# Kernel optimization log

Measured on AMD Instinct MI355X. Metric: run time of the kernel, lower is better.

Reference implementation:

```python
import jax, jax.numpy as jnp
import numpy as np

PASSES = 6
S = 2           # numEdgeSets
D = 256         # inputLayerSize
OUT = 10        # outputLayerSize
HID = 80
B, N, E = 4, 10000, 160000


def _leaky(x):
    return jax.nn.leaky_relu(x, negative_slope=0.01)


def setup_inputs() -> dict:
    key = jax.random.key(0)
    ks = jax.random.split(key, 18)
    sc = 0.05
    return {
        "nodes": jax.random.normal(ks[0], (B, N, D), jnp.float32),
        "edges": jax.random.randint(ks[1], (B, S, E, 2), 0, N, jnp.int32),
        "problem_type": jax.random.uniform(ks[2], (B, 1), jnp.float32),
        # GRUCell params (torch layout: [3D, D] for ih and hh)
        "gru_w_ih": jax.random.normal(ks[3], (3 * D, D), jnp.float32) * sc,
        "gru_w_hh": jax.random.normal(ks[4], (3 * D, D), jnp.float32) * sc,
        "gru_b_ih": jax.random.normal(ks[5], (3 * D,), jnp.float32) * sc,
        "gru_b_hh": jax.random.normal(ks[6], (3 * D,), jnp.float32) * sc,
        # per-edge-set 2-layer MLP, stacked over edge sets
        "edge_w1": jax.random.normal(ks[7], (S, D, D), jnp.float32) * sc,
        "edge_b1": jax.random.normal(ks[8], (S, D), jnp.float32) * sc,
        "edge_w2": jax.random.normal(ks[9], (S, D, D), jnp.float32) * sc,
        "edge_b2": jax.random.normal(ks[10], (S, D), jnp.float32) * sc,
        # readout head
        "fc1_w": jax.random.normal(ks[11], (HID, D + 1), jnp.float32) * sc,
        "fc1_b": jax.random.normal(ks[12], (HID,), jnp.float32) * sc,
        "fc2_w": jax.random.normal(ks[13], (HID, HID), jnp.float32) * sc,
        "fc2_b": jax.random.normal(ks[14], (HID,), jnp.float32) * sc,
        "fc3_w": jax.random.normal(ks[15], (OUT, HID), jnp.float32) * sc,
        "fc3_b": jax.random.normal(ks[16], (OUT,), jnp.float32) * sc,
    }


def _gru_cell(x, h, w_ih, w_hh, b_ih, b_hh):
    # torch.nn.GRUCell semantics; x,h: [B,N,D]
    gi = jnp.einsum("bnd,ed->bne", x, w_ih) + b_ih   # [B,N,3D]
    gh = jnp.einsum("bnd,ed->bne", h, w_hh) + b_hh
    i_r, i_z, i_n = jnp.split(gi, 3, axis=-1)
    h_r, h_z, h_n = jnp.split(gh, 3, axis=-1)
    r = jax.nn.sigmoid(i_r + h_r)
    z = jax.nn.sigmoid(i_z + h_z)
    n = jnp.tanh(i_n + r * h_n)
    return (1.0 - z) * n + z * h


def reference(nodes, edges, problem_type, gru_w_ih, gru_w_hh, gru_b_ih, gru_b_hh,
              edge_w1, edge_b1, edge_w2, edge_b2,
              fc1_w, fc1_b, fc2_w, fc2_b, fc3_w, fc3_b):
    bidx = jnp.arange(B)[:, None]  # [B,1] for batched scatter
    h = nodes
    for j in range(PASSES):
        incoming = jnp.zeros_like(h)
        for si in range(S):
            dst = edges[:, si, :, 0]  # [B,E]
            src = edges[:, si, :, 1]  # [B,E]
            gathered = jnp.take_along_axis(h, src[:, :, None], axis=1)  # [B,E,D]
            y = _leaky(jnp.einsum("bed,fd->bef", gathered, edge_w1[si]) + edge_b1[si])
            y = jnp.einsum("bed,fd->bef", y, edge_w2[si]) + edge_b2[si]
            incoming = incoming.at[bidx, dst].add(y)
        h = _gru_cell(incoming, h, gru_w_ih, gru_w_hh, gru_b_ih, gru_b_hh)
        if j < PASSES - 2:
            h = jax.lax.stop_gradient(h)  # mirrors .detach()
    # graph readout: sum over nodes, log, nan->0, relu, +inf->finite max
    s = jnp.sum(h, axis=1)               # [B,D]
    l = jnp.log(s)
    l = jnp.where(jnp.isnan(l), 0.0, l)
    l = jax.nn.relu(l)
    finite_max = jnp.max(jnp.where(jnp.isinf(l), -jnp.inf, l), axis=1, keepdims=True)
    l = jnp.where(jnp.isinf(l), finite_max, l)
    x = jnp.concatenate([l, problem_type], axis=1)  # [B,D+1]
    x = _leaky(x @ fc1_w.T + fc1_b)
    x = _leaky(x @ fc2_w.T + fc2_b)
    return x @ fc3_w.T + fc3_b  # [B,OUT]
```

## Files before the change

### kernel.cpp

```cpp
#include <hip/hip_runtime.h>
#include <math.h>

#define NNODES 10000
#define NEDGES 160000
#define DIM    256
#define BATCH  4
#define NG     8
#define MROWS  40064
#define RBLK   625
#define RGRP   79
#define RBLK128 313
#define RGRP128 40

typedef __attribute__((ext_vector_type(8))) __bf16 bf16x8;
typedef __attribute__((ext_vector_type(4))) float  floatx4;
typedef __attribute__((ext_vector_type(8))) unsigned short ushort8v;

__device__ __forceinline__ float leakyf(float x){ return x > 0.f ? x : 0.01f*x; }
__device__ __forceinline__ float fsig(float x){ return 1.f/(1.f + __expf(-x)); }
__device__ __forceinline__ float ftanh(float x){ return 1.f - 2.f/(1.f + __expf(2.f*x)); }
__device__ __forceinline__ unsigned short f2bf_u(float x){
  unsigned int u = __float_as_uint(x);
  u += 0x7fffu + ((u >> 16) & 1u);
  return (unsigned short)(u >> 16);
}
__device__ __forceinline__ float bfdec(unsigned short u){
  return __uint_as_float(((unsigned int)u) << 16);
}
#define GATE_SCL 65535.f
#define GATE_INV 1.5259021896696422e-5f

__device__ __forceinline__ void glds16(unsigned short* lds, const unsigned short* g){
  __builtin_amdgcn_global_load_lds(
      (const __attribute__((address_space(1))) void*)g,
      (__attribute__((address_space(3))) void*)lds, 16, 0, 0);
}

__global__ void ihinit_kernel(const float* __restrict__ nodes,
                              unsigned short* __restrict__ ihcat,
                              unsigned short* __restrict__ h_lo){
  int idx = blockIdx.x*256 + threadIdx.x;
  int row = idx >> 8, d = idx & 255;
  float v = nodes[idx];
  unsigned short h = f2bf_u(v);
  ihcat[(size_t)row*512 + 256 + d] = h;
  h_lo[idx] = f2bf_u(v - bfdec(h));
}

__global__ void w1cat_kernel(const float* __restrict__ ew1, unsigned short* __restrict__ o){
  int idx = blockIdx.x*256 + threadIdx.x;
  int n = idx >> 8, k = idx & 255;
  o[idx] = f2bf_u(ew1[(n>>8)*65536 + (n&255)*256 + k]);
}
__global__ void w2k_kernel(const float* __restrict__ ew2, unsigned short* __restrict__ o){
  int idx = blockIdx.x*256 + threadIdx.x;
  int n = idx >> 10, kp = idx & 1023;
  int j = kp & 511, term = kp >> 9;
  int si = j >> 8, k = j & 255;
  float v = ew2[si*65536 + n*256 + k];
  unsigned short h = f2bf_u(v);
  o[idx] = term ? f2bf_u(v - bfdec(h)) : h;
}
__global__ void wk2_kernel(const float* __restrict__ w, unsigned short* __restrict__ o){
  int idx = blockIdx.x*256 + threadIdx.x;
  int c = idx >> 9, kp = idx & 511;
  int k = kp & 255, term = kp >> 8;
  float v = w[c*256 + k];
  unsigned short h = f2bf_u(v);
  o[idx] = term ? f2bf_u(v - bfdec(h)) : h;
}
__global__ void wcomb_kernel(const float* __restrict__ wih, const float* __restrict__ whh,
                             unsigned short* __restrict__ o){
  int idx = blockIdx.x*256 + threadIdx.x;
  int c = idx >> 10, kp = idx & 1023;
  int seg = kp >> 8, k = kp & 255;
  const float* w = (seg & 1) ? whh : wih;
  float v = w[c*256 + k];
  unsigned short h = f2bf_u(v);
  o[idx] = (seg >> 1) ? f2bf_u(v - bfdec(h)) : h;
}

__global__ void hist_kernel(const int* __restrict__ edges, int* __restrict__ cnt){
  int idx = blockIdx.x*256 + threadIdx.x;
  if (idx < NG*NEDGES){
    int g = idx / NEDGES, e = idx - g*NEDGES;
    int d = edges[((size_t)g*NEDGES + e)*2];
    atomicAdd(&cnt[g*NNODES + d], 1);
  }
}

__global__ __launch_bounds__(256) void scan_kernel(const int* __restrict__ cnt, int* __restrict__ off){
  __shared__ int sc[256];
  int g = blockIdx.x, t = threadIdx.x;
  int base = 0;
  for (int c=0;c<40;c++){
    int i = c*256 + t;
    int v = (i < NNODES) ? cnt[g*NNODES + i] : 0;
    __syncthreads();
    sc[t] = v;
    __syncthreads();
    for (int o=1;o<256;o<<=1){
      int u = (t>=o) ? sc[t-o] : 0;
      __syncthreads();
      sc[t] += u;
      __syncthreads();
    }
    if (i < NNODES) off[g*(NNODES+1) + i] = base + sc[t] - v;
    base += sc[255];
  }
  if (t == 0) off[g*(NNODES+1) + NNODES] = base;
}

__global__ void scatter_kernel(const int* __restrict__ edges, const int* __restrict__ off,
                               int* __restrict__ cur, int* __restrict__ ssrc){
  int idx = blockIdx.x*256 + threadIdx.x;
  if (idx < NG*NEDGES){
    int g = idx / NEDGES, e = idx - g*NEDGES;
    const int* ep = &edges[((size_t)g*NEDGES + e)*2];
    int d = ep[0], s = ep[1];
    int pos = off[g*(NNODES+1) + d] + atomicAdd(&cur[g*NNODES + d], 1);
    ssrc[g*NEDGES + pos] = s;
  }
}

template<int KP, int RS, int KM>
__device__ __forceinline__ void mm64_core(
    const unsigned short* __restrict__ Ab, const unsigned short* __restrict__ Wb,
    unsigned short* lds, floatx4 (&acc)[4][2])
{
  const int t = threadIdx.x;
  const int w = t >> 6, lane = t & 63;
  const int q = lane >> 4, col = lane & 15;
  const int wc = w*32;

  const int sr = t >> 3;
  const int sj = t & 7;
  const int sk = ((sj ^ (sr & 7)) * 8);

  {
    unsigned short* Al = lds;
    unsigned short* Bl = lds + 4096;
    #pragma unroll
    for (int i=0;i<2;i++){
      int r = i*32 + sr;
      glds16(&Al[i*2048 + w*512], &Ab[(size_t)r*RS + (sk & KM)]);
    }
    #pragma unroll
    for (int i=0;i<4;i++){
      int r = i*32 + sr;
      glds16(&Bl[i*2048 + w*512], &Wb[(size_t)r*KP + sk]);
    }
  }
  __syncthreads();
  int cur = 0;
  for (int kb = 0; kb < KP; kb += 64){
    if (kb + 64 < KP){
      unsigned short* Al = lds + (cur^1)*12288;
      unsigned short* Bl = Al + 4096;
      int kn = kb + 64;
      #pragma unroll
      for (int i=0;i<2;i++){
        int r = i*32 + sr;
        glds16(&Al[i*2048 + w*512], &Ab[(size_t)r*RS + ((kn + sk) & KM)]);
      }
      #pragma unroll
      for (int i=0;i<4;i++){
        int r = i*32 + sr;
        glds16(&Bl[i*2048 + w*512], &Wb[(size_t)r*KP + kn + sk]);
      }
    }
    const unsigned short* Al = lds + cur*12288;
    const unsigned short* Bl = Al + 4096;
    #pragma unroll
    for (int ks2=0; ks2<2; ks2++){
      bf16x8 a[4], bf[2];
      #pragma unroll
      for (int mi=0;mi<4;mi++){
        int r = mi*16 + col;
        int j = (ks2*4 + q) ^ (r & 7);
        a[mi] = *(const bf16x8*)&Al[r*64 + j*8];
      }
      #pragma unroll
      for (int ni=0;ni<2;ni++){
        int r = wc + ni*16 + col;
        int j = (ks2*4 + q) ^ (r & 7);
        bf[ni] = *(const bf16x8*)&Bl[r*64 + j*8];
      }
      #pragma unroll
      for (int mi=0;mi<4;mi++)
        #pragma unroll
        for (int ni=0;ni<2;ni++)
          acc[mi][ni] = __builtin_amdgcn_mfma_f32_16x16x32_bf16(a[mi], bf[ni], acc[mi][ni], 0,0,0);
    }
    __syncthreads();
    cur ^= 1;
  }
}

template<int KP, int RS, int KM>
__device__ __forceinline__ void mm128_core(
    const unsigned short* __restrict__ Ab, const unsigned short* __restrict__ Wb,
    unsigned short* lds, floatx4 (&acc)[4][4])
{
  const int t = threadIdx.x;
  const int w = t >> 6, lane = t & 63;
  const int q = lane >> 4, col = lane & 15;
  const int wr = (w >> 1) * 64;
  const int wc = (w & 1) * 64;

  const int sr = t >> 3;
  const int sj = t & 7;
  const int sk = ((sj ^ (sr & 7)) * 8);

  {
    unsigned short* Al = lds;
    unsigned short* Bl = lds + 8192;
    #pragma unroll
    for (int i=0;i<4;i++){
      int r = i*32 + sr;
      glds16(&Al[i*2048 + w*512], &Ab[(size_t)r*RS + (sk & KM)]);
      glds16(&Bl[i*2048 + w*512], &Wb[(size_t)r*KP + sk]);
    }
  }
  __syncthreads();
  int cur = 0;
  for (int kb = 0; kb < KP; kb += 64){
    if (kb + 64 < KP){
      unsigned short* Al = lds + (cur^1)*16384;
      unsigned short* Bl = Al + 8192;
      int kn = kb + 64;
      #pragma unroll
      for (int i=0;i<4;i++){
        int r = i*32 + sr;
        glds16(&Al[i*2048 + w*512], &Ab[(size_t)r*RS + ((kn + sk) & KM)]);
        glds16(&Bl[i*2048 + w*512], &Wb[(size_t)r*KP + kn + sk]);
      }
    }
    const unsigned short* Al = lds + cur*16384;
    const unsigned short* Bl = Al + 8192;
    #pragma unroll
    for (int ks2=0; ks2<2; ks2++){
      bf16x8 a[4], bf[4];
      #pragma unroll
      for (int mi=0;mi<4;mi++){
        int r = wr + mi*16 + col;
        int j = (ks2*4 + q) ^ (r & 7);
        a[mi] = *(const bf16x8*)&Al[r*64 + j*8];
      }
      #pragma unroll
      for (int ni=0;ni<4;ni++){
        int r = wc + ni*16 + col;
        int j = (ks2*4 + q) ^ (r & 7);
        bf[ni] = *(const bf16x8*)&Bl[r*64 + j*8];
      }
      #pragma unroll
      for (int mi=0;mi<4;mi++)
        #pragma unroll
        for (int ni=0;ni<4;ni++)
          acc[mi][ni] = __builtin_amdgcn_mfma_f32_16x16x32_bf16(a[mi], bf[ni], acc[mi][ni], 0,0,0);
    }
    __syncthreads();
    cur ^= 1;
  }
}

#define XDECODE(NCOL) \
  const int bid_ = blockIdx.x; \
  const int rb_ = ((bid_ >> 3) / NCOL) * 8 + (bid_ & 7); \
  const int colb_ = (bid_ >> 3) % NCOL; \
  if (rb_ >= RBLK) return;

#define XDECODE128(NCOL) \
  const int bid_ = blockIdx.x; \
  const int rb_ = ((bid_ >> 3) / NCOL) * 8 + (bid_ & 7); \
  const int colb_ = (bid_ >> 3) % NCOL; \
  if (rb_ >= RBLK128) return;

#define MMPRO \
  const int t = threadIdx.x, w = t >> 6, lane = t & 63; \
  const int q = lane >> 4, col = lane & 15; \
  const int wc = w*32; \
  floatx4 acc[4][2]; \
  _Pragma("unroll") for (int mi=0;mi<4;mi++) _Pragma("unroll") for (int ni=0;ni<2;ni++) \
    acc[mi][ni] = (floatx4){0.f,0.f,0.f,0.f};

#define MMPRO128 \
  const int t = threadIdx.x, w = t >> 6, lane = t & 63; \
  const int q = lane >> 4, col = lane & 15; \
  const int wrq = (w >> 1) * 64, wcq = (w & 1) * 64; \
  floatx4 acc[4][4]; \
  _Pragma("unroll") for (int mi=0;mi<4;mi++) _Pragma("unroll") for (int ni=0;ni<4;ni++) \
    acc[mi][ni] = (floatx4){0.f,0.f,0.f,0.f};

__global__ __launch_bounds__(256) void z64_kernel(
    const unsigned short* __restrict__ ihcat, const unsigned short* __restrict__ w1cat,
    const float* __restrict__ eb1, unsigned short* __restrict__ Z)
{
  __shared__ unsigned short lds[32768];
  XDECODE128(4)
  const int row0 = rb_*128, col0 = colb_*128;
  MMPRO128
  mm128_core<256,512,255>(ihcat + (size_t)row0*512 + 256, w1cat + (size_t)col0*256, lds, acc);

  #pragma unroll
  for (int ni=0;ni<4;ni++){
    int n = col0 + wcq + ni*16 + col;
    int si = n >> 8, cz = n & 255;
    float bb = eb1[si*256 + cz];
    unsigned short* zp = Z + (size_t)si*MROWS*256 + cz;
    #pragma unroll
    for (int mi=0;mi<4;mi++)
      #pragma unroll
      for (int rr=0;rr<4;rr++){
        int row = row0 + wrq + mi*16 + q*4 + rr;
        zp[(size_t)row*256] = f2bf_u(leakyf(acc[mi][ni][rr] + bb));
      }
  }
}

__global__ __launch_bounds__(256) void aggregate_kernel(
    const unsigned short* __restrict__ Z, const int* __restrict__ ssrc,
    const int* __restrict__ off, unsigned short* __restrict__ Sb)
{
  const int bid = blockIdx.x;
  const int g = bid & 7;
  const int dgrp = bid >> 3;
  const int b = g >> 1, si = g & 1;
  const int w = threadIdx.x >> 6, lane = threadIdx.x & 63;
  const int half = lane >> 5, c = lane & 31;
  const unsigned short* zb = Z + ((size_t)si*MROWS + b*10000)*256 + c*8;
  const int* sp = ssrc + (size_t)g*NEDGES;
  const int* offg = off + g*(NNODES+1);

  #pragma unroll
  for (int p=0;p<2;p++){
    const int d = dgrp*16 + w*4 + p*2 + half;
    int j = offg[d];
    const int j1 = offg[d+1];
    float a0=0.f,a1=0.f,a2=0.f,a3=0.f,a4=0.f,a5=0.f,a6=0.f,a7=0.f;
    for (; j+8 <= j1; j+=8){
      int s[8];
      #pragma unroll
      for (int e=0;e<8;e++) s[e] = sp[j+e];
      ushort8v u[8];
      #pragma unroll
      for (int e=0;e<8;e++) u[e] = *(const ushort8v*)&zb[(size_t)s[e]*256];
      a0 += bfdec(u[0][0])+bfdec(u[1][0])+bfdec(u[2][0])+bfdec(u[3][0]);
      a1 += bfdec(u[0][1])+bfdec(u[1][1])+bfdec(u[2][1])+bfdec(u[3][1]);
      a2 += bfdec(u[0][2])+bfdec(u[1][2])+bfdec(u[2][2])+bfdec(u[3][2]);
      a3 += bfdec(u[0][3])+bfdec(u[1][3])+bfdec(u[2][3])+bfdec(u[3][3]);
      a4 += bfdec(u[0][4])+bfdec(u[1][4])+bfdec(u[2][4])+bfdec(u[3][4]);
      a5 += bfdec(u[0][5])+bfdec(u[1][5])+bfdec(u[2][5])+bfdec(u[3][5]);
      a6 += bfdec(u[0][6])+bfdec(u[1][6])+bfdec(u[2][6])+bfdec(u[3][6]);
      a7 += bfdec(u[0][7])+bfdec(u[1][7])+bfdec(u[2][7])+bfdec(u[3][7]);
      a0 += bfdec(u[4][0])+bfdec(u[5][0])+bfdec(u[6][0])+bfdec(u[7][0]);
      a1 += bfdec(u[4][1])+bfdec(u[5][1])+bfdec(u[6][1])+bfdec(u[7][1]);
      a2 += bfdec(u[4][2])+bfdec(u[5][2])+bfdec(u[6][2])+bfdec(u[7][2]);
      a3 += bfdec(u[4][3])+bfdec(u[5][3])+bfdec(u[6][3])+bfdec(u[7][3]);
      a4 += bfdec(u[4][4])+bfdec(u[5][4])+bfdec(u[6][4])+bfdec(u[7][4]);
      a5 += bfdec(u[4][5])+bfdec(u[5][5])+bfdec(u[6][5])+bfdec(u[7][5]);
      a6 += bfdec(u[4][6])+bfdec(u[5][6])+bfdec(u[6][6])+bfdec(u[7][6]);
      a7 += bfdec(u[4][7])+bfdec(u[5][7])+bfdec(u[6][7])+bfdec(u[7][7]);
    }
    for (; j+4 <= j1; j+=4){
      int s0=sp[j], s1=sp[j+1], s2=sp[j+2], s3=sp[j+3];
      ushort8v u0 = *(const ushort8v*)&zb[(size_t)s0*256];
      ushort8v u1 = *(const ushort8v*)&zb[(size_t)s1*256];
      ushort8v u2 = *(const ushort8v*)&zb[(size_t)s2*256];
      ushort8v u3 = *(const ushort8v*)&zb[(size_t)s3*256];
      a0 += bfdec(u0[0])+bfdec(u1[0])+bfdec(u2[0])+bfdec(u3[0]);
      a1 += bfdec(u0[1])+bfdec(u1[1])+bfdec(u2[1])+bfdec(u3[1]);
      a2 += bfdec(u0[2])+bfdec(u1[2])+bfdec(u2[2])+bfdec(u3[2]);
      a3 += bfdec(u0[3])+bfdec(u1[3])+bfdec(u2[3])+bfdec(u3[3]);
      a4 += bfdec(u0[4])+bfdec(u1[4])+bfdec(u2[4])+bfdec(u3[4]);
      a5 += bfdec(u0[5])+bfdec(u1[5])+bfdec(u2[5])+bfdec(u3[5]);
      a6 += bfdec(u0[6])+bfdec(u1[6])+bfdec(u2[6])+bfdec(u3[6]);
      a7 += bfdec(u0[7])+bfdec(u1[7])+bfdec(u2[7])+bfdec(u3[7]);
    }
    for (; j < j1; j++){
      ushort8v u = *(const ushort8v*)&zb[(size_t)sp[j]*256];
      a0+=bfdec(u[0]); a1+=bfdec(u[1]); a2+=bfdec(u[2]); a3+=bfdec(u[3]);
      a4+=bfdec(u[4]); a5+=bfdec(u[5]); a6+=bfdec(u[6]); a7+=bfdec(u[7]);
    }
    size_t so = (size_t)(b*10000 + d)*512 + si*256 + c*8;
    ushort8v hv;
    hv[0]=f2bf_u(a0); hv[1]=f2bf_u(a1); hv[2]=f2bf_u(a2); hv[3]=f2bf_u(a3);
    hv[4]=f2bf_u(a4); hv[5]=f2bf_u(a5); hv[6]=f2bf_u(a6); hv[7]=f2bf_u(a7);
    *(ushort8v*)&Sb[so] = hv;
  }
}

__global__ __launch_bounds__(256) void w264_kernel(
    const unsigned short* __restrict__ Sb, const unsigned short* __restrict__ w2k,
    const float* __restrict__ eb2, const int* __restrict__ off,
    unsigned short* __restrict__ ihcat)
{
  __shared__ unsigned short lds[32768];
  XDECODE128(2)
  const int row0 = rb_*128, col0 = colb_*128;
  MMPRO128
  mm128_core<1024,512,511>(Sb + (size_t)row0*512, w2k + (size_t)col0*1024, lds, acc);

  float b20[4], b21[4];
  #pragma unroll
  for (int ni=0;ni<4;ni++){
    int n = col0 + wcq + ni*16 + col;
    b20[ni] = eb2[n];
    b21[ni] = eb2[256 + n];
  }
  #pragma unroll
  for (int mi=0;mi<4;mi++)
    #pragma unroll
    for (int rr=0;rr<4;rr++){
      int row = row0 + wrq + mi*16 + q*4 + rr;
      int rw = (row < 40000) ? row : 39999;
      int b = rw / 10000, d = rw - b*10000;
      int o0 = (b*2)*(NNODES+1) + d;
      int o1 = (b*2+1)*(NNODES+1) + d;
      float dg0 = (float)(off[o0+1] - off[o0]);
      float dg1 = (float)(off[o1+1] - off[o1]);
      #pragma unroll
      for (int ni=0;ni<4;ni++){
        int n = col0 + wcq + ni*16 + col;
        ihcat[(size_t)row*512 + n] = f2bf_u(acc[mi][ni][rr] + dg0*b20[ni] + dg1*b21[ni]);
      }
    }
}

__global__ __launch_bounds__(256) void gruA_kernel(
    const unsigned short* __restrict__ ihcat, const unsigned short* __restrict__ wcomb,
    const float* __restrict__ b_ih, const float* __restrict__ b_hh,
    unsigned short* __restrict__ rz_r, unsigned short* __restrict__ rz_z)
{
  __shared__ unsigned short lds[32768];
  XDECODE128(4)
  const int row0 = rb_*128, col0 = colb_*128;
  MMPRO128
  mm128_core<1024,512,511>(ihcat + (size_t)row0*512, wcomb + (size_t)col0*1024, lds, acc);

  float bb[4];
  #pragma unroll
  for (int ni=0;ni<4;ni++){
    int n = col0 + wcq + ni*16 + col;
    bb[ni] = b_ih[n] + b_hh[n];
  }
  unsigned short* dst = (col0 < 256) ? rz_r : rz_z;
  const int cbase = (col0 & 255) + wcq;
  #pragma unroll
  for (int mi=0;mi<4;mi++)
    #pragma unroll
    for (int rr=0;rr<4;rr++){
      size_t row = (size_t)(row0 + wrq + mi*16 + q*4 + rr);
      #pragma unroll
      for (int ni=0;ni<4;ni++){
        float v = fsig(acc[mi][ni][rr] + bb[ni]);
        dst[row*256 + cbase + ni*16 + col] = (unsigned short)(v*GATE_SCL + 0.5f);
      }
    }
}

__global__ __launch_bounds__(256) void gruB_kernel(
    const unsigned short* __restrict__ ihcat, unsigned short* __restrict__ h_lo,
    const unsigned short* __restrict__ wihk, const unsigned short* __restrict__ whhk,
    const float* __restrict__ b_ih, const float* __restrict__ b_hh,
    const unsigned short* __restrict__ rz_r, const unsigned short* __restrict__ rz_z,
    unsigned short* __restrict__ ihcat_nxt)
{
  __shared__ unsigned short lds[24576];
  XDECODE(2)
  const int row0 = rb_*64, dcol0 = colb_*128;
  const int t = threadIdx.x, w = t >> 6, lane = t & 63;
  const int q = lane >> 4, col = lane & 15;
  const int wc = w*32;

  floatx4 ai[4][2], ah[4][2];
  #pragma unroll
  for (int mi=0;mi<4;mi++)
    #pragma unroll
    for (int ni=0;ni<2;ni++){ ai[mi][ni] = (floatx4){0.f,0.f,0.f,0.f}; ah[mi][ni] = (floatx4){0.f,0.f,0.f,0.f}; }

  mm64_core<512,512,255>(ihcat + (size_t)row0*512,       wihk + (size_t)(512 + dcol0)*512, lds, ai);
  mm64_core<512,512,255>(ihcat + (size_t)row0*512 + 256, whhk + (size_t)(512 + dcol0)*512, lds, ah);

  float bi[2], bh[2];
  #pragma unroll
  for (int ni=0;ni<2;ni++){
    int n = 512 + dcol0 + wc + ni*16 + col;
    bi[ni] = b_ih[n]; bh[ni] = b_hh[n];
  }
  #pragma unroll
  for (int mi=0;mi<4;mi++)
    #pragma unroll
    for (int rr=0;rr<4;rr++){
      size_t row = (size_t)(row0 + mi*16 + q*4 + rr);
      #pragma unroll
      for (int ni=0;ni<2;ni++){
        int dn = dcol0 + wc + ni*16 + col;
        float rg = (float)rz_r[row*256 + dn] * GATE_INV;
        float zg = (float)rz_z[row*256 + dn] * GATE_INV;
        float ng = ftanh(ai[mi][ni][rr] + bi[ni] + rg*(ah[mi][ni][rr] + bh[ni]));
        float hv = bfdec(ihcat[row*512 + 256 + dn]) + bfdec(h_lo[row*256 + dn]);
        float hnew = (1.f - zg)*ng + zg*hv;
        unsigned short hh = f2bf_u(hnew);
        ihcat_nxt[row*512 + 256 + dn] = hh;
        h_lo[row*256 + dn] = f2bf_u(hnew - bfdec(hh));
      }
    }
}

__global__ void reduce_kernel(const unsigned short* __restrict__ ihcat,
                              const unsigned short* __restrict__ h_lo,
                              float* __restrict__ sbuf){
  int b  = blockIdx.x / 50;
  int s0 = (blockIdx.x % 50) * 200;
  int d  = threadIdx.x;
  size_t row = (size_t)b*NNODES + s0;
  float acc = 0.f;
  for (int i=0;i<200;i++){
    acc += bfdec(ihcat[(row+i)*512 + 256 + d]) + bfdec(h_lo[(row+i)*256 + d]);
  }
  atomicAdd(&sbuf[b*DIM + d], acc);
}

__global__ __launch_bounds__(320) void head_kernel(
    const float* __restrict__ sbuf, const float* __restrict__ pt,
    const float* __restrict__ fc1w, const float* __restrict__ fc1b,
    const float* __restrict__ fc2w, const float* __restrict__ fc2b,
    const float* __restrict__ fc3w, const float* __restrict__ fc3b,
    float* __restrict__ out)
{
  __shared__ float L[4][257];
  __shared__ float T1[4][80];
  __shared__ float T2[4][80];
  __shared__ float fmx[4];
  int t = threadIdx.x;
  if (t < 256){
    for (int b=0;b<4;b++){
      float v = sbuf[b*DIM + t];
      float ll = logf(v);
      if (ll != ll) ll = 0.f;
      ll = fmaxf(ll, 0.f);
      L[b][t] = ll;
    }
  }
  __syncthreads();
  int w = t >> 6, lane = t & 63;
  if (w < 4){
    float m = -INFINITY;
    for (int i=lane;i<256;i+=64){ float v = L[w][i]; if (v != INFINITY) m = fmaxf(m, v); }
    #pragma unroll
    for (int o=32;o>=1;o>>=1) m = fmaxf(m, __shfl_xor(m, o, 64));
    if (lane==0) fmx[w] = m;
  }
  __syncthreads();
  if (t < 256){
    for (int b=0;b<4;b++) if (L[b][t] == INFINITY) L[b][t] = fmx[b];
  }
  if (t < 4) L[t][256] = pt[t];
  __syncthreads();
  if (t < 320){
    int b = t/80, i = t%80;
    float a = fc1b[i];
    for (int k=0;k<257;k++) a += L[b][k]*fc1w[i*257+k];
    T1[b][i] = leakyf(a);
  }
  __syncthreads();
  if (t < 320){
    int b = t/80, i = t%80;
    float a = fc2b[i];
    for (int k=0;k<80;k++) a += T1[b][k]*fc2w[i*80+k];
    T2[b][i] = leakyf(a);
  }
  __syncthreads();
  if (t < 40){
    int b = t/10, i = t%10;
    float a = fc3b[i];
    for (int k=0;k<80;k++) a += T2[b][k]*fc3w[i*80+k];
    out[b*10+i] = a;
  }
}

extern "C" void kernel_launch(void* const* d_in, const int* in_sizes, int n_in,
                              void* d_out, int out_size, void* d_ws, size_t ws_size,
                              hipStream_t stream) {
  const float* nodes = (const float*)d_in[0];
  const int*   edges = (const int*)d_in[1];
  const float* pt    = (const float*)d_in[2];
  const float* w_ih  = (const float*)d_in[3];
  const float* w_hh  = (const float*)d_in[4];
  const float* b_ih  = (const float*)d_in[5];
  const float* b_hh  = (const float*)d_in[6];
  const float* ew1   = (const float*)d_in[7];
  const float* eb1   = (const float*)d_in[8];
  const float* ew2   = (const float*)d_in[9];
  const float* eb2   = (const float*)d_in[10];
  const float* fc1w  = (const float*)d_in[11];
  const float* fc1b  = (const float*)d_in[12];
  const float* fc2w  = (const float*)d_in[13];
  const float* fc2b  = (const float*)d_in[14];
  const float* fc3w  = (const float*)d_in[15];
  const float* fc3b  = (const float*)d_in[16];

  const size_t HN  = (size_t)BATCH*NNODES*DIM;
  const size_t HNP = (size_t)MROWS*DIM;
  char* p = (char*)d_ws;
  float* sbuf = (float*)p;                        p += BATCH*DIM*4;
  unsigned short* ihcat0 = (unsigned short*)p;    p += (size_t)MROWS*512*2;
  unsigned short* ihcat1 = (unsigned short*)p;    p += (size_t)MROWS*512*2;
  unsigned short* h_lo   = (unsigned short*)p;    p += HNP*2;
  unsigned short* Zb   = (unsigned short*)p;      p += 2*HNP*2;
  unsigned short* Sb   = (unsigned short*)p;      p += (size_t)MROWS*512*2;
  unsigned short* w1cat= (unsigned short*)p;      p += 512*256*2;
  unsigned short* w2k  = (unsigned short*)p;      p += 256*1024*2;
  unsigned short* wihk = (unsigned short*)p;      p += 768*512*2;
  unsigned short* whhk = (unsigned short*)p;      p += 768*512*2;
  unsigned short* wcomb= (unsigned short*)p;      p += 512*1024*2;
  int* off  = (int*)p;                            p += NG*(NNODES+1)*4;
  int* cur  = (int*)p;                            p += NG*NNODES*4;
  int* ssrc = (int*)p;                            p += (size_t)NG*NEDGES*4;

  unsigned short* rz_r = (unsigned short*)Sb;
  unsigned short* rz_z = rz_r + (size_t)MROWS*256;

  w1cat_kernel<<<512,256,0,stream>>>(ew1, w1cat);
  w2k_kernel<<<1024,256,0,stream>>>(ew2, w2k);
  wk2_kernel<<<1536,256,0,stream>>>(w_ih, wihk);
  wk2_kernel<<<1536,256,0,stream>>>(w_hh, whhk);
  wcomb_kernel<<<2048,256,0,stream>>>(w_ih, w_hh, wcomb);

  ihinit_kernel<<<(int)(HN/256),256,0,stream>>>(nodes, ihcat0, h_lo);

  hipMemsetAsync(cur, 0, NG*NNODES*sizeof(int), stream);
  hist_kernel<<<(NG*NEDGES)/256,256,0,stream>>>(edges, cur);
  scan_kernel<<<NG,256,0,stream>>>(cur, off);
  hipMemsetAsync(cur, 0, NG*NNODES*sizeof(int), stream);
  scatter_kernel<<<(NG*NEDGES)/256,256,0,stream>>>(edges, off, cur, ssrc);

  hipMemsetAsync(sbuf, 0, BATCH*DIM*sizeof(float), stream);

  unsigned short* ih[2] = {ihcat0, ihcat1};

  for (int pass=0; pass<6; pass++){
    unsigned short* curb = ih[pass & 1];
    unsigned short* nxtb = ih[(pass+1) & 1];
    z64_kernel<<<RGRP128*8*4,256,0,stream>>>(curb, w1cat, eb1, Zb);
    aggregate_kernel<<<5000,256,0,stream>>>(Zb, ssrc, off, Sb);
    w264_kernel<<<RGRP128*8*2,256,0,stream>>>(Sb, w2k, eb2, off, curb);
    gruA_kernel<<<RGRP128*8*4,256,0,stream>>>(curb, wcomb, b_ih, b_hh, rz_r, rz_z);
    gruB_kernel<<<RGRP*8*2,256,0,stream>>>(curb, h_lo, wihk, whhk, b_ih, b_hh,
                                           rz_r, rz_z, nxtb);
  }
  reduce_kernel<<<200,256,0,stream>>>(ih[0], h_lo, sbuf);
  head_kernel<<<1,320,0,stream>>>(sbuf, pt, fc1w,fc1b,fc2w,fc2b,fc3w,fc3b,(float*)d_out);
}
```

Measured before the change: 1.702 ms.

## Use fine-grained vmcnt waits and merge the two GRU n-gate GEMMs into one pipeline

```diff
diff --git a/kernel.cpp b/kernel.cpp
--- a/kernel.cpp
+++ b/kernel.cpp
@@ -29,6 +29,13 @@
 }
 #define GATE_SCL 65535.f
 #define GATE_INV 1.5259021896696422e-5f
+
+#define VMCNT8 asm volatile("s_waitcnt vmcnt(8)" ::: "memory")
+#define VMCNT6 asm volatile("s_waitcnt vmcnt(6)" ::: "memory")
+#define VMCNT0 asm volatile("s_waitcnt vmcnt(0)" ::: "memory")
+#define LGKM0  asm volatile("s_waitcnt lgkmcnt(0)" ::: "memory")
+#define SBAR   __builtin_amdgcn_s_barrier()
+#define SCHEDB __builtin_amdgcn_sched_barrier(0)
 
 __device__ __forceinline__ void glds16(unsigned short* lds, const unsigned short* g){
   __builtin_amdgcn_global_load_lds(
@@ -124,80 +131,6 @@
 }
 
 template<int KP, int RS, int KM>
-__device__ __forceinline__ void mm64_core(
-    const unsigned short* __restrict__ Ab, const unsigned short* __restrict__ Wb,
-    unsigned short* lds, floatx4 (&acc)[4][2])
-{
-  const int t = threadIdx.x;
-  const int w = t >> 6, lane = t & 63;
-  const int q = lane >> 4, col = lane & 15;
-  const int wc = w*32;
-
-  const int sr = t >> 3;
-  const int sj = t & 7;
-  const int sk = ((sj ^ (sr & 7)) * 8);
-
-  {
-    unsigned short* Al = lds;
-    unsigned short* Bl = lds + 4096;
-    #pragma unroll
-    for (int i=0;i<2;i++){
-      int r = i*32 + sr;
-      glds16(&Al[i*2048 + w*512], &Ab[(size_t)r*RS + (sk & KM)]);
-    }
-    #pragma unroll
-    for (int i=0;i<4;i++){
-      int r = i*32 + sr;
-      glds16(&Bl[i*2048 + w*512], &Wb[(size_t)r*KP + sk]);
-    }
-  }
-  __syncthreads();
-  int cur = 0;
-  for (int kb = 0; kb < KP; kb += 64){
-    if (kb + 64 < KP){
-      unsigned short* Al = lds + (cur^1)*12288;
-      unsigned short* Bl = Al + 4096;
-      int kn = kb + 64;
-      #pragma unroll
-      for (int i=0;i<2;i++){
-        int r = i*32 + sr;
-        glds16(&Al[i*2048 + w*512], &Ab[(size_t)r*RS + ((kn + sk) & KM)]);
-      }
-      #pragma unroll
-      for (int i=0;i<4;i++){
-        int r = i*32 + sr;
-        glds16(&Bl[i*2048 + w*512], &Wb[(size_t)r*KP + kn + sk]);
-      }
-    }
-    const unsigned short* Al = lds + cur*12288;
-    const unsigned short* Bl = Al + 4096;
-    #pragma unroll
-    for (int ks2=0; ks2<2; ks2++){
-      bf16x8 a[4], bf[2];
-      #pragma unroll
-      for (int mi=0;mi<4;mi++){
-        int r = mi*16 + col;
-        int j = (ks2*4 + q) ^ (r & 7);
-        a[mi] = *(const bf16x8*)&Al[r*64 + j*8];
-      }
-      #pragma unroll
-      for (int ni=0;ni<2;ni++){
-        int r = wc + ni*16 + col;
-        int j = (ks2*4 + q) ^ (r & 7);
-        bf[ni] = *(const bf16x8*)&Bl[r*64 + j*8];
-      }
-      #pragma unroll
-      for (int mi=0;mi<4;mi++)
-        #pragma unroll
-        for (int ni=0;ni<2;ni++)
-          acc[mi][ni] = __builtin_amdgcn_mfma_f32_16x16x32_bf16(a[mi], bf[ni], acc[mi][ni], 0,0,0);
-    }
-    __syncthreads();
-    cur ^= 1;
-  }
-}
-
-template<int KP, int RS, int KM>
 __device__ __forceinline__ void mm128_core(
     const unsigned short* __restrict__ Ab, const unsigned short* __restrict__ Wb,
     unsigned short* lds, floatx4 (&acc)[4][4])
@@ -207,35 +140,31 @@
   const int q = lane >> 4, col = lane & 15;
   const int wr = (w >> 1) * 64;
   const int wc = (w & 1) * 64;
-
   const int sr = t >> 3;
-  const int sj = t & 7;
-  const int sk = ((sj ^ (sr & 7)) * 8);
-
-  {
-    unsigned short* Al = lds;
-    unsigned short* Bl = lds + 8192;
+  const int sk = ((t & 7) ^ (sr & 7)) * 8;
+
+  auto STAGE = [&](int kb, int buf){
+    unsigned short* Al = lds + buf*16384;
+    unsigned short* Bl = Al + 8192;
     #pragma unroll
     for (int i=0;i<4;i++){
       int r = i*32 + sr;
-      glds16(&Al[i*2048 + w*512], &Ab[(size_t)r*RS + (sk & KM)]);
-      glds16(&Bl[i*2048 + w*512], &Wb[(size_t)r*KP + sk]);
-    }
-  }
-  __syncthreads();
+      glds16(&Al[i*2048 + w*512], &Ab[(size_t)r*RS + ((kb + sk) & KM)]);
+      glds16(&Bl[i*2048 + w*512], &Wb[(size_t)r*KP + kb + sk]);
+    }
+  };
+
+  STAGE(0, 0);
   int cur = 0;
+  #pragma unroll
   for (int kb = 0; kb < KP; kb += 64){
     if (kb + 64 < KP){
-      unsigned short* Al = lds + (cur^1)*16384;
-      unsigned short* Bl = Al + 8192;
-      int kn = kb + 64;
-      #pragma unroll
-      for (int i=0;i<4;i++){
-        int r = i*32 + sr;
-        glds16(&Al[i*2048 + w*512], &Ab[(size_t)r*RS + ((kn + sk) & KM)]);
-        glds16(&Bl[i*2048 + w*512], &Wb[(size_t)r*KP + kn + sk]);
-      }
-    }
+      STAGE(kb + 64, cur^1);
+      VMCNT8;
+    } else {
+      VMCNT0;
+    }
+    SBAR; SCHEDB;
     const unsigned short* Al = lds + cur*16384;
     const unsigned short* Bl = Al + 8192;
     #pragma unroll
@@ -259,7 +188,84 @@
         for (int ni=0;ni<4;ni++)
           acc[mi][ni] = __builtin_amdgcn_mfma_f32_16x16x32_bf16(a[mi], bf[ni], acc[mi][ni], 0,0,0);
     }
-    __syncthreads();
+    SCHEDB; LGKM0; SBAR;
+    cur ^= 1;
+  }
+}
+
+__device__ __forceinline__ void mm64x2_core(
+    const unsigned short* __restrict__ A1, const unsigned short* __restrict__ W1,
+    const unsigned short* __restrict__ A2, const unsigned short* __restrict__ W2,
+    unsigned short* lds, floatx4 (&ai)[4][2], floatx4 (&ah)[4][2])
+{
+  const int t = threadIdx.x;
+  const int w = t >> 6, lane = t & 63;
+  const int q = lane >> 4, col = lane & 15;
+  const int wc = w*32;
+  const int sr = t >> 3;
+  const int sk = ((t & 7) ^ (sr & 7)) * 8;
+
+  auto STAGE = [&](int s, int buf){
+    const unsigned short* A = (s < 8) ? A1 : A2;
+    const unsigned short* W = (s < 8) ? W1 : W2;
+    int kb = (s & 7) * 64;
+    unsigned short* Al = lds + buf*12288;
+    unsigned short* Bl = Al + 4096;
+    #pragma unroll
+    for (int i=0;i<2;i++){
+      int r = i*32 + sr;
+      glds16(&Al[i*2048 + w*512], &A[(size_t)r*512 + ((kb + sk) & 255)]);
+    }
+    #pragma unroll
+    for (int i=0;i<4;i++){
+      int r = i*32 + sr;
+      glds16(&Bl[i*2048 + w*512], &W[(size_t)r*512 + kb + sk]);
+    }
+  };
+
+  STAGE(0, 0);
+  int cur = 0;
+  #pragma unroll
+  for (int s = 0; s < 16; s++){
+    if (s < 15){
+      STAGE(s + 1, cur^1);
+      VMCNT6;
+    } else {
+      VMCNT0;
+    }
+    SBAR; SCHEDB;
+    const unsigned short* Al = lds + cur*12288;
+    const unsigned short* Bl = Al + 4096;
+    #pragma unroll
+    for (int ks2=0; ks2<2; ks2++){
+      bf16x8 a[4], bf[2];
+      #pragma unroll
+      for (int mi=0;mi<4;mi++){
+        int r = mi*16 + col;
+        int j = (ks2*4 + q) ^ (r & 7);
+        a[mi] = *(const bf16x8*)&Al[r*64 + j*8];
+      }
+      #pragma unroll
+      for (int ni=0;ni<2;ni++){
+        int r = wc + ni*16 + col;
+        int j = (ks2*4 + q) ^ (r & 7);
+        bf[ni] = *(const bf16x8*)&Bl[r*64 + j*8];
+      }
+      if (s < 8){
+        #pragma unroll
+        for (int mi=0;mi<4;mi++)
+          #pragma unroll
+          for (int ni=0;ni<2;ni++)
+            ai[mi][ni] = __builtin_amdgcn_mfma_f32_16x16x32_bf16(a[mi], bf[ni], ai[mi][ni], 0,0,0);
+      } else {
+        #pragma unroll
+        for (int mi=0;mi<4;mi++)
+          #pragma unroll
+          for (int ni=0;ni<2;ni++)
+            ah[mi][ni] = __builtin_amdgcn_mfma_f32_16x16x32_bf16(a[mi], bf[ni], ah[mi][ni], 0,0,0);
+      }
+    }
+    SCHEDB; LGKM0; SBAR;
     cur ^= 1;
   }
 }
@@ -275,14 +281,6 @@
   const int rb_ = ((bid_ >> 3) / NCOL) * 8 + (bid_ & 7); \
   const int colb_ = (bid_ >> 3) % NCOL; \
   if (rb_ >= RBLK128) return;
-
-#define MMPRO \
-  const int t = threadIdx.x, w = t >> 6, lane = t & 63; \
-  const int q = lane >> 4, col = lane & 15; \
-  const int wc = w*32; \
-  floatx4 acc[4][2]; \
-  _Pragma("unroll") for (int mi=0;mi<4;mi++) _Pragma("unroll") for (int ni=0;ni<2;ni++) \
-    acc[mi][ni] = (floatx4){0.f,0.f,0.f,0.f};
 
 #define MMPRO128 \
   const int t = threadIdx.x, w = t >> 6, lane = t & 63; \
@@ -479,8 +477,9 @@
     #pragma unroll
     for (int ni=0;ni<2;ni++){ ai[mi][ni] = (floatx4){0.f,0.f,0.f,0.f}; ah[mi][ni] = (floatx4){0.f,0.f,0.f,0.f}; }
 
-  mm64_core<512,512,255>(ihcat + (size_t)row0*512,       wihk + (size_t)(512 + dcol0)*512, lds, ai);
-  mm64_core<512,512,255>(ihcat + (size_t)row0*512 + 256, whhk + (size_t)(512 + dcol0)*512, lds, ah);
+  mm64x2_core(ihcat + (size_t)row0*512,       wihk + (size_t)(512 + dcol0)*512,
+              ihcat + (size_t)row0*512 + 256, whhk + (size_t)(512 + dcol0)*512,
+              lds, ai, ah);
 
   float bi[2], bh[2];
   #pragma unroll
```

After: 1.670 ms. About the same (-1.8%).
